# Optimization experiments

Measured on AMD Instinct MI355X. Metric: run time of the kernel, lower is better.

Reference implementation:

```python
import jax, jax.numpy as jnp
import numpy as np

EPS = 1e-08


def setup_inputs() -> dict:
    key = jax.random.key(0)
    B, D = 8192, 512
    student_output = jax.random.normal(key, (B, D), dtype=jnp.float32)
    return {"student_output": student_output}


def reference(student_output) -> jnp.ndarray:
    # F.normalize(p=2, dim=-1, eps=EPS): x / max(||x||, eps)
    norm = jnp.linalg.norm(student_output, axis=-1, keepdims=True)
    x = student_output / jnp.maximum(norm, EPS)

    n = x.shape[0]
    # Pairwise inner products; mask the diagonal with -1 (self-match)
    dots = jnp.matmul(x, x.T)  # [B, B]
    idx = jnp.arange(n)
    dots = dots.at[idx, idx].set(-1.0)
    I = jnp.argmax(dots, axis=1)  # nearest neighbor index per row

    # torch.nn.PairwiseDistance(2, eps): ||x1 - x2 + eps||_2
    diff = x - x[I] + EPS
    distances = jnp.linalg.norm(diff, axis=-1)  # [B]
    loss = -jnp.mean(jnp.log(distances + EPS))
    return loss
```

## Files before the change

### kernel.cpp

```cpp
#include <hip/hip_runtime.h>
#include <hip/hip_bf16.h>
#include <math.h>

#define D_DIM 512
#define TM    128
#define TN    256
#define BK    128

typedef int i32x4 __attribute__((ext_vector_type(4)));
typedef unsigned long long u64;


__device__ inline u64 shfl_xor_u64(u64 x, int m) {
    int lo = __shfl_xor((int)(unsigned)(x & 0xFFFFFFFFull), m, 64);
    int hi = __shfl_xor((int)(unsigned)(x >> 32), m, 64);
    return ((u64)(unsigned)hi << 32) | (u64)(unsigned)lo;
}

__device__ inline void async16(unsigned char* lds, const unsigned char* g) {
    __builtin_amdgcn_global_load_lds(
        (const __attribute__((address_space(1))) void*)g,
        (__attribute__((address_space(3))) void*)lds,
        16, 0, 0);
}


__global__ __launch_bounds__(256) void normalize_rows(
        const float* __restrict__ in, unsigned char* __restrict__ xb,
        float* __restrict__ inv_norm, u64* __restrict__ best,
        float* __restrict__ acc, int* __restrict__ cnt) {
    const int row  = blockIdx.x * 4 + (threadIdx.x >> 6);
    const int lane = threadIdx.x & 63;
    if (blockIdx.x == 0 && threadIdx.x == 0) { acc[0] = 0.f; cnt[0] = 0; }
    const float4* rp = (const float4*)(in + (size_t)row * D_DIM) + lane * 2;
    float4 a = rp[0], b = rp[1];
    float s = a.x*a.x + a.y*a.y + a.z*a.z + a.w*a.w
            + b.x*b.x + b.y*b.y + b.z*b.z + b.w*b.w;
    #pragma unroll
    for (int m = 1; m <= 32; m <<= 1) s += __shfl_xor(s, m, 64);
    float inv = 1.0f / fmaxf(sqrtf(s), 1e-8f);
    if (lane == 0) {
        inv_norm[row] = inv;
        best[row] = 0ull;
    }
    float sc = inv * 127.0f;
    int q0 = __float2int_rn(a.x*sc), q1 = __float2int_rn(a.y*sc);
    int q2 = __float2int_rn(a.z*sc), q3 = __float2int_rn(a.w*sc);
    int q4 = __float2int_rn(b.x*sc), q5 = __float2int_rn(b.y*sc);
    int q6 = __float2int_rn(b.z*sc), q7 = __float2int_rn(b.w*sc);
    int lo = (q0 & 255) | ((q1 & 255) << 8) | ((q2 & 255) << 16) | ((q3 & 255) << 24);
    int hi = (q4 & 255) | ((q5 & 255) << 8) | ((q6 & 255) << 16) | ((q7 & 255) << 24);
    ((int2*)(xb + (size_t)row * D_DIM))[lane] = make_int2(lo, hi);
}


__global__ __launch_bounds__(256, 2) void gemm_argmax(
        const unsigned char* __restrict__ X, u64* __restrict__ best) {
    __shared__ unsigned char As[TM * BK];
    __shared__ unsigned char Bs[TN * BK];
    __shared__ u64 rmerge[TM * 2];
    __shared__ u64 cmerge[TN * 2];

    int l = blockIdx.x;
    int q = (int)(sqrtf((float)l / 16.0f + 0.25f) - 0.5f);
    while (16 * (q + 1) * (q + 2) <= l) ++q;
    while (16 * q * (q + 1) > l) --q;
    int rrem = l - 16 * q * (q + 1);
    int cw   = 8 * (q + 1);
    int c    = rrem / cw;
    int bi   = rrem - c * cw;
    int bj   = 4 * q + c;
    if (bi > 2 * bj + 1) return;
    const int m0 = bi * TM;
    const int n0 = bj * TN;

    const int t    = threadIdx.x;
    const int lane = t & 63;
    const int w    = t >> 6;
    const int wm   = w >> 1, wn = w & 1;
    const int qr   = lane & 15;
    const int quad = lane >> 4;

    const int rS   = t >> 3;
    const int gSrc = ((t & 7) ^ ((t >> 3) & 7)) * 16;
    const unsigned char* gA = X + (size_t)(m0 + rS) * D_DIM + gSrc;
    const unsigned char* gB = X + (size_t)(n0 + rS) * D_DIM + gSrc;

    i32x4 accm[4][8];
    #pragma unroll
    for (int mi = 0; mi < 4; mi++)
        #pragma unroll
        for (int ni = 0; ni < 8; ni++)
            accm[mi][ni] = (i32x4){0, 0, 0, 0};

    for (int k0 = 0; k0 < D_DIM; k0 += BK) {
        #pragma unroll
        for (int j = 0; j < 4; j++)
            async16(As + j * 4096 + t * 16, gA + (size_t)(j * 32) * D_DIM + k0);
        #pragma unroll
        for (int j = 0; j < 8; j++)
            async16(Bs + j * 4096 + t * 16, gB + (size_t)(j * 32) * D_DIM + k0);
        __syncthreads();

        #pragma unroll
        for (int ks = 0; ks < 2; ks++) {
            i32x4 av[4], bv[8];
            #pragma unroll
            for (int mi = 0; mi < 4; mi++) {
                int r   = wm * 64 + mi * 16 + qr;
                int pos = (ks * 4 + quad) ^ (r & 7);
                av[mi] = *(const i32x4*)(As + r * BK + pos * 16);
            }
            #pragma unroll
            for (int ni = 0; ni < 8; ni++) {
                int r   = wn * 128 + ni * 16 + qr;
                int pos = (ks * 4 + quad) ^ (r & 7);
                bv[ni] = *(const i32x4*)(Bs + r * BK + pos * 16);
            }
            #pragma unroll
            for (int mi = 0; mi < 4; mi++)
                #pragma unroll
                for (int ni = 0; ni < 8; ni++)
                    accm[mi][ni] = __builtin_amdgcn_mfma_i32_16x16x64_i8(
                        av[mi], bv[ni], accm[mi][ni], 0, 0, 0);
        }
        __syncthreads();
    }

    const int colg_base = n0 + wn * 128 + qr;
    #pragma unroll
    for (int mi = 0; mi < 4; mi++) {
        #pragma unroll
        for (int r = 0; r < 4; r++) {
            const int rowl = wm * 64 + mi * 16 + quad * 4 + r;
            const int rowg = m0 + rowl;
            u64 key = 0ull;
            #pragma unroll
            for (int ni = 0; ni < 8; ni++) {
                int colg = colg_base + ni * 16;
                if (colg == rowg) continue;
                unsigned bd = (unsigned)accm[mi][ni][r] + 0x80000000u;
                u64 k = ((u64)bd << 32) | (u64)(0xFFFFFFFFu - (unsigned)colg);
                key = key > k ? key : k;
            }
            #pragma unroll
            for (int m = 1; m <= 8; m <<= 1) {
                u64 o = shfl_xor_u64(key, m);
                key = key > o ? key : o;
            }
            if (qr == 0) rmerge[rowl * 2 + wn] = key;
        }
    }

    #pragma unroll
    for (int ni = 0; ni < 8; ni++) {
        const int colg = colg_base + ni * 16;
        u64 key = 0ull;
        #pragma unroll
        for (int mi = 0; mi < 4; mi++) {
            #pragma unroll
            for (int r = 0; r < 4; r++) {
                int rowg = m0 + wm * 64 + mi * 16 + quad * 4 + r;
                if (rowg == colg) continue;
                unsigned bd = (unsigned)accm[mi][ni][r] + 0x80000000u;
                u64 k = ((u64)bd << 32) | (u64)(0xFFFFFFFFu - (unsigned)rowg);
                key = key > k ? key : k;
            }
        }
        u64 o = shfl_xor_u64(key, 16); key = key > o ? key : o;
        o     = shfl_xor_u64(key, 32); key = key > o ? key : o;
        if (quad == 0) cmerge[(wn * 128 + ni * 16 + qr) * 2 + wm] = key;
    }
    __syncthreads();
    if (t < TM) {
        u64 a = rmerge[t * 2], b = rmerge[t * 2 + 1];
        u64 k = a > b ? a : b;
        atomicMax(&best[m0 + t], k);
    }
    {
        u64 ca = cmerge[t * 2], cb = cmerge[t * 2 + 1];
        u64 ck = ca > cb ? ca : cb;
        atomicMax(&best[n0 + t], ck);
    }
}


__global__ __launch_bounds__(256) void neighbor_reduce(
        const float* __restrict__ in, const float* __restrict__ inv_norm,
        const u64* __restrict__ best, float* __restrict__ acc,
        int* __restrict__ cnt, float* __restrict__ out, int B) {
    const int wave = threadIdx.x >> 6;
    const int lane = threadIdx.x & 63;
    float lsum = 0.f;
    #pragma unroll
    for (int rr = 0; rr < 8; rr++) {
        const int row = blockIdx.x * 32 + wave * 8 + rr;
        u64 k   = best[row];
        int nbr = (int)(0xFFFFFFFFu - (unsigned)(k & 0xFFFFFFFFull));
        float ir  = inv_norm[row];
        float inb = inv_norm[nbr];
        const float4* rp = (const float4*)(in + (size_t)row * D_DIM) + lane * 2;
        const float4* np = (const float4*)(in + (size_t)nbr * D_DIM) + lane * 2;
        float4 r0 = rp[0], r1 = rp[1], q0 = np[0], q1 = np[1];
        float d0 = r0.x*ir - q0.x*inb + 1e-8f, d1 = r0.y*ir - q0.y*inb + 1e-8f;
        float d2 = r0.z*ir - q0.z*inb + 1e-8f, d3 = r0.w*ir - q0.w*inb + 1e-8f;
        float d4 = r1.x*ir - q1.x*inb + 1e-8f, d5 = r1.y*ir - q1.y*inb + 1e-8f;
        float d6 = r1.z*ir - q1.z*inb + 1e-8f, d7 = r1.w*ir - q1.w*inb + 1e-8f;
        float s = d0*d0 + d1*d1 + d2*d2 + d3*d3 + d4*d4 + d5*d5 + d6*d6 + d7*d7;
        #pragma unroll
        for (int m = 1; m <= 32; m <<= 1) s += __shfl_xor(s, m, 64);
        if (lane == 0) lsum += logf(sqrtf(s) + 1e-8f);
    }
    __shared__ float sb[4];
    if (lane == 0) sb[wave] = lsum;
    __syncthreads();
    if (threadIdx.x == 0) {
        float partial = sb[0] + sb[1] + sb[2] + sb[3];
        atomicAdd(acc, partial);
        __threadfence();
        int done = atomicAdd(cnt, 1);
        if (done == gridDim.x - 1) {
            __threadfence();
            float tot = atomicAdd(acc, 0.0f);
            out[0] = -tot / (float)B;
        }
    }
}


extern "C" void kernel_launch(void* const* d_in, const int* in_sizes, int n_in,
                              void* d_out, int out_size, void* d_ws, size_t ws_size,
                              hipStream_t stream) {
    const float* in = (const float*)d_in[0];
    const int B = in_sizes[0] / D_DIM;
    const int nblk = 16 * 8 * 9;

    char* w = (char*)d_ws;
    unsigned char* xb = (unsigned char*)w;
    float* invn = (float*)(w + (size_t)B * D_DIM);
    u64*   best = (u64*)(w + (size_t)B * D_DIM + (size_t)B * 4);
    float* acc  = (float*)(w + (size_t)B * D_DIM + (size_t)B * 4 + (size_t)B * 8);
    int*   cnt  = (int*)(acc + 1);
    float* out  = (float*)d_out;

    normalize_rows<<<B / 4, 256, 0, stream>>>(in, xb, invn, best, acc, cnt);
    gemm_argmax<<<nblk, 256, 0, stream>>>(xb, best);
    neighbor_reduce<<<B / 32, 256, 0, stream>>>(in, invn, best, acc, cnt, out, B);
}
```

Measured before the change: 116.4 us.

## Load GEMM operands directly from global memory into registers, dropping LDS staging

Removes the shared-memory tiles and async global-to-LDS copies in the int8 GEMM-argmax kernel. Each wave now loads its MFMA fragments straight from global memory (the 4 MB int8 matrix fits in cache), with the full K loop unrolled and no barriers. This removes LDS traffic and synchronisation, but loads shared between waves are now duplicated through L2/L1 and the 16-byte row-strided accesses are poorly coalesced.

After: 158.5 us. 1.36x slower.

```diff
diff --git a/kernel.cpp b/kernel.cpp
--- a/kernel.cpp
+++ b/kernel.cpp
@@ -5,7 +5,6 @@
 #define D_DIM 512
 #define TM    128
 #define TN    256
-#define BK    128
 
 typedef int i32x4 __attribute__((ext_vector_type(4)));
 typedef unsigned long long u64;
@@ -15,13 +14,6 @@
     int lo = __shfl_xor((int)(unsigned)(x & 0xFFFFFFFFull), m, 64);
     int hi = __shfl_xor((int)(unsigned)(x >> 32), m, 64);
     return ((u64)(unsigned)hi << 32) | (u64)(unsigned)lo;
-}
-
-__device__ inline void async16(unsigned char* lds, const unsigned char* g) {
-    __builtin_amdgcn_global_load_lds(
-        (const __attribute__((address_space(1))) void*)g,
-        (__attribute__((address_space(3))) void*)lds,
-        16, 0, 0);
 }
 
 
@@ -56,8 +48,6 @@
 
 __global__ __launch_bounds__(256, 2) void gemm_argmax(
         const unsigned char* __restrict__ X, u64* __restrict__ best) {
-    __shared__ unsigned char As[TM * BK];
-    __shared__ unsigned char Bs[TN * BK];
     __shared__ u64 rmerge[TM * 2];
     __shared__ u64 cmerge[TN * 2];
 
@@ -81,10 +71,13 @@
     const int qr   = lane & 15;
     const int quad = lane >> 4;
 
-    const int rS   = t >> 3;
-    const int gSrc = ((t & 7) ^ ((t >> 3) & 7)) * 16;
-    const unsigned char* gA = X + (size_t)(m0 + rS) * D_DIM + gSrc;
-    const unsigned char* gB = X + (size_t)(n0 + rS) * D_DIM + gSrc;
+    int offA[4], offB[8];
+    #pragma unroll
+    for (int mi = 0; mi < 4; mi++)
+        offA[mi] = (m0 + wm * 64 + mi * 16 + qr) * D_DIM + quad * 16;
+    #pragma unroll
+    for (int ni = 0; ni < 8; ni++)
+        offB[ni] = (n0 + wn * 128 + ni * 16 + qr) * D_DIM + quad * 16;
 
     i32x4 accm[4][8];
     #pragma unroll
@@ -93,38 +86,21 @@
         for (int ni = 0; ni < 8; ni++)
             accm[mi][ni] = (i32x4){0, 0, 0, 0};
 
-    for (int k0 = 0; k0 < D_DIM; k0 += BK) {
-        #pragma unroll
-        for (int j = 0; j < 4; j++)
-            async16(As + j * 4096 + t * 16, gA + (size_t)(j * 32) * D_DIM + k0);
-        #pragma unroll
-        for (int j = 0; j < 8; j++)
-            async16(Bs + j * 4096 + t * 16, gB + (size_t)(j * 32) * D_DIM + k0);
-        __syncthreads();
-
-        #pragma unroll
-        for (int ks = 0; ks < 2; ks++) {
-            i32x4 av[4], bv[8];
-            #pragma unroll
-            for (int mi = 0; mi < 4; mi++) {
-                int r   = wm * 64 + mi * 16 + qr;
-                int pos = (ks * 4 + quad) ^ (r & 7);
-                av[mi] = *(const i32x4*)(As + r * BK + pos * 16);
-            }
-            #pragma unroll
-            for (int ni = 0; ni < 8; ni++) {
-                int r   = wn * 128 + ni * 16 + qr;
-                int pos = (ks * 4 + quad) ^ (r & 7);
-                bv[ni] = *(const i32x4*)(Bs + r * BK + pos * 16);
-            }
-            #pragma unroll
-            for (int mi = 0; mi < 4; mi++)
-                #pragma unroll
-                for (int ni = 0; ni < 8; ni++)
-                    accm[mi][ni] = __builtin_amdgcn_mfma_i32_16x16x64_i8(
-                        av[mi], bv[ni], accm[mi][ni], 0, 0, 0);
-        }
-        __syncthreads();
+    #pragma unroll
+    for (int k0 = 0; k0 < D_DIM; k0 += 64) {
+        i32x4 av[4], bv[8];
+        #pragma unroll
+        for (int mi = 0; mi < 4; mi++)
+            av[mi] = *(const i32x4*)(X + offA[mi] + k0);
+        #pragma unroll
+        for (int ni = 0; ni < 8; ni++)
+            bv[ni] = *(const i32x4*)(X + offB[ni] + k0);
+        #pragma unroll
+        for (int mi = 0; mi < 4; mi++)
+            #pragma unroll
+            for (int ni = 0; ni < 8; ni++)
+                accm[mi][ni] = __builtin_amdgcn_mfma_i32_16x16x64_i8(
+                    av[mi], bv[ni], accm[mi][ni], 0, 0, 0);
     }
 
     const int colg_base = n0 + wn * 128 + qr;
```
